# Kernel tuning notes

Measured on AMD Instinct MI355X. Metric: run time of the kernel, lower is better.

Reference implementation:

```python
import jax, jax.numpy as jnp
import numpy as np

STRIDE = 2
PADDING = 1


def setup_inputs() -> dict:
    key = jax.random.key(0)
    k1, k2, k3, k4, k5 = jax.random.split(key, 5)
    B, C, H, W = 32, 128, 64, 64
    O, kh, kw = 256, 3, 3
    ah = H + 2 * PADDING - (kh - 1)  # 64
    oh = ah // STRIDE                # 32 (divisible -> ceil == floor, rest == 0)
    inputs = {
        "input": jax.random.normal(k1, (B, C, H, W), dtype=jnp.float32),
        "weight": jax.random.normal(k2, (O, C, kh, kw), dtype=jnp.float32) * 0.05,
        "bias": jax.random.normal(k3, (O,), dtype=jnp.float32) * 0.05,
        "selh": jax.random.randint(k4, (oh, oh), 0, STRIDE, dtype=jnp.int32),
        "selw": jax.random.randint(k5, (oh, oh), 0, STRIDE, dtype=jnp.int32),
    }
    return inputs


def reference(input, weight, bias, selh, selw):
    # Faithful to SConv2dAvg.forward with stoch=True, mask == -1, stride=2:
    # unfold(input, k, pad, stride=1) -> stochastic gather of one position per
    # stride x stride cell (offsets selh/selw) -> GEMM with flattened weight -> reshape.
    B, C, H, W = input.shape
    O, _, kh, kw = weight.shape
    ah = H + 2 * PADDING - (kh - 1)
    aw = W + 2 * PADDING - (kw - 1)
    oh = ah // STRIDE  # divisible by construction; ceil_mode correction is a no-op
    ow = aw // STRIDE
    xp = jnp.pad(input, ((0, 0), (0, 0), (PADDING, PADDING), (PADDING, PADDING)))
    # selected unfold positions in the afterconv grid
    rng_h = selh + (jnp.arange(oh, dtype=selh.dtype) * STRIDE)[:, None]   # [oh, ow]
    rng_w = selw + (jnp.arange(ow, dtype=selw.dtype) * STRIDE)[None, :]   # [oh, ow]
    # gather k x k patches directly (equivalent to gathering unfold columns)
    rows = rng_h[:, :, None, None] + jnp.arange(kh)[None, None, :, None]  # [oh, ow, kh, 1]
    cols = rng_w[:, :, None, None] + jnp.arange(kw)[None, None, None, :]  # [oh, ow, 1, kw]
    patches = xp[:, :, rows, cols]  # [B, C, oh, ow, kh, kw]
    out = jnp.einsum('bchwij,ocij->bohw', patches, weight) + bias[None, :, None, None]
    return out  # [B, O, oh, ow]
```

## Files before the change

### kernel.cpp

```cpp
#include <hip/hip_runtime.h>
#include <hip/hip_bf16.h>


typedef short bf16x8 __attribute__((ext_vector_type(8)));
typedef float f32x4  __attribute__((ext_vector_type(4)));

#define KSTEPS 18
#define WPRE_BYTES (KSTEPS * 256 * 64 * 2)
#define TRANS_BYTES (32 * 66 * 66 * 128 * 2)
#define TOTAL_WS (WPRE_BYTES + TRANS_BYTES)

__device__ __forceinline__ unsigned short f2bf(float x) {
  unsigned u = __float_as_uint(x);
  return (unsigned short)((u + 0x7fffu + ((u >> 16) & 1u)) >> 16);
}
__device__ __forceinline__ unsigned pk2(float a, float b) {
  unsigned ua = __float_as_uint(a), ub = __float_as_uint(b);
  return ((ua + 0x7fffu + ((ua >> 16) & 1u)) >> 16) |
         ((ub + 0x7fffu + ((ub >> 16) & 1u)) & 0xffff0000u);
}
__device__ __forceinline__ bf16x8 ld_frag(const uint4* a) {
  union { uint4 u; bf16x8 s; } cv; cv.u = *a; return cv.s;
}
__device__ __forceinline__ void async16(const void* g, void* l) {
  __builtin_amdgcn_global_load_lds(
      (__attribute__((address_space(1))) void*)(void*)g,
      (__attribute__((address_space(3))) void*)l, 16, 0, 0);
}

__global__ __launch_bounds__(256) void wprep(const float* __restrict__ w,
                                             unsigned short* __restrict__ wpre) {
  int idx = (blockIdx.x << 8) + threadIdx.x;
  if (idx >= KSTEPS * 16384) return;
  int k_in = idx & 63;
  int o    = (idx >> 6) & 255;
  int kk   = idx >> 14;
  int kg   = (kk << 6) + (k_in ^ ((o & 7) << 3));
  int tap  = kg >> 7;
  int c    = kg & 127;
  int di   = (tap >= 6) ? 2 : ((tap >= 3) ? 1 : 0);
  int dj   = tap - di * 3;
  wpre[idx] = f2bf(w[(o * 128 + c) * 9 + di * 3 + dj]);
}

__global__ __launch_bounds__(256) void transform(const float* __restrict__ in,
                                                 unsigned short* __restrict__ tp) {
  __shared__ float lds[128 * 65];
  const int hp  = blockIdx.x;
  const int b   = blockIdx.y;
  const int tid = threadIdx.x;
  uint4* rowp = (uint4*)(tp + (size_t)(b * 66 + hp) * 66 * 128);
  uint4 z; z.x = z.y = z.z = z.w = 0u;
  if (hp == 0 || hp == 65) {
    for (int s = tid; s < 1056; s += 256) rowp[s] = z;
    return;
  }
  const int h = hp - 1;
  const float* src = in + ((size_t)b << 19) + (h << 6);
  const int w = tid & 63, c0 = tid >> 6;
#pragma unroll
  for (int pass = 0; pass < 32; ++pass) {
    int c = (pass << 2) + c0;
    lds[c * 65 + w] = src[((size_t)c << 12) + w];
  }
  __syncthreads();
  for (int s = tid; s < 1056; s += 256) {
    if (s < 16 || s >= 1040) { rowp[s] = z; continue; }
    int idx = s - 16;
    int wq = idx >> 4, c8 = idx & 15;
    const float* lp = lds + (c8 << 3) * 65 + wq;
    uint4 d;
    d.x = pk2(lp[0],   lp[65]);
    d.y = pk2(lp[130], lp[195]);
    d.z = pk2(lp[260], lp[325]);
    d.w = pk2(lp[390], lp[455]);
    rowp[s] = d;
  }
}

__global__ __launch_bounds__(512, 4) void sconv_mfma2(
    const unsigned short* __restrict__ tp,
    const unsigned short* __restrict__ wpre,
    const float* __restrict__ bias,
    const int* __restrict__ selh,
    const int* __restrict__ selw,
    float* __restrict__ out)
{
  __shared__ uint4 Alds[128 * 8];
  __shared__ uint4 Blds[128 * 8];
  __shared__ float bias_s[128];

  const int tid   = threadIdx.x;
  const int blk   = blockIdx.x;
  const int b     = blk >> 4;
  const int y0    = ((blk >> 1) & 7) << 2;
  const int ohalf = blk & 1;

  if (tid < 128) bias_s[tid] = bias[(ohalf << 7) + tid];

  const int p0 = tid >> 3;
  const int sl = tid & 7;
  int addr0, addr1;
  {
    const int py0 = y0 + (p0 >> 5);
    const int px  = p0 & 31;
    const int sh0 = selh[(py0 << 5) | px], sw0 = selw[(py0 << 5) | px];
    const int py1 = py0 + 2;
    const int sh1 = selh[(py1 << 5) | px], sw1 = selw[(py1 << 5) | px];
    addr0 = (b * 66 + 2 * py0 + sh0) * 66 + 2 * px + sw0;
    addr1 = (b * 66 + 2 * py1 + sh1) * 66 + 2 * px + sw1;
  }
  const int n0 = sl ^ (p0 & 7);
  const char* tbase = (const char*)tp;

  const int wv = tid >> 6, ln = tid & 63;
  const int wo = wv & 1;
  const int wp = wv >> 1;
  const int lo = ln & 15, hi = ln >> 4;

  const char* wsrc = (const char*)wpre + (ohalf << 14) + (tid << 4);

  f32x4 acc[4][2] = {};

  for (int kk = 0; kk < KSTEPS; ++kk) {
    const int tap = kk >> 1;
    const int di  = (tap >= 6) ? 2 : ((tap >= 3) ? 1 : 0);
    const int dj  = tap - 3 * di;
    const int toff = ((di * 66 + dj) << 8) + ((kk & 1) << 7) + (n0 << 4);

    async16(tbase + ((size_t)addr0 << 8) + toff, Alds + (wv << 6));
    async16(tbase + ((size_t)addr1 << 8) + toff, Alds + (wv << 6) + 512);
    async16(wsrc + (kk << 15),        Blds + (wv << 6));
    async16(wsrc + (kk << 15) + 8192, Blds + (wv << 6) + 512);

    __syncthreads();

    bf16x8 FW[4][2], FP[2][2];
#pragma unroll
    for (int f = 0; f < 4; ++f) {
      const int orow = (wo << 6) + (f << 4) + lo;
#pragma unroll
      for (int ks = 0; ks < 2; ++ks)
        FW[f][ks] = ld_frag(Blds + (orow << 3) + (((ks << 2) | hi) ^ (orow & 7)));
    }
#pragma unroll
    for (int f = 0; f < 2; ++f) {
      const int prow = (wp << 5) + (f << 4) + lo;
#pragma unroll
      for (int ks = 0; ks < 2; ++ks)
        FP[f][ks] = ld_frag(Alds + (prow << 3) + (((ks << 2) | hi) ^ (prow & 7)));
    }
#pragma unroll
    for (int fo = 0; fo < 4; ++fo)
#pragma unroll
      for (int fp = 0; fp < 2; ++fp)
#pragma unroll
        for (int ks = 0; ks < 2; ++ks)
          acc[fo][fp] = __builtin_amdgcn_mfma_f32_16x16x32_bf16(
              FW[fo][ks], FP[fp][ks], acc[fo][fp], 0, 0, 0);

    __syncthreads();
  }

  float* ob = out + ((size_t)b << 18) + ((size_t)ohalf << 17) + (y0 << 5);
#pragma unroll
  for (int fo = 0; fo < 4; ++fo) {
    const int obase = (wo << 6) + (fo << 4) + (hi << 2);
#pragma unroll
    for (int fp = 0; fp < 2; ++fp) {
      const int pix = (wp << 5) + (fp << 4) + lo;
#pragma unroll
      for (int j = 0; j < 4; ++j) {
        const int o = obase + j;
        ob[((size_t)o << 10) + pix] = acc[fo][fp][j] + bias_s[o];
      }
    }
  }
}

__global__ __launch_bounds__(512, 2) void sconv_mfma(
    const float* __restrict__ in, const unsigned short* __restrict__ wpre,
    const float* __restrict__ bias, const int* __restrict__ selh,
    const int* __restrict__ selw, float* __restrict__ out) {
  __shared__ uint4 Alds[128 * 8];
  __shared__ uint4 Blds[256 * 8];
  __shared__ float bias_s[256];
  const int tid = threadIdx.x;
  const int blk = blockIdx.x;
  const int b   = blk >> 3;
  const int y0  = (blk & 7) << 2;
  if (tid < 256) bias_s[tid] = bias[tid];
  const int p    = tid & 127;
  const int csub = tid >> 7;
  const int py   = y0 + (p >> 5);
  const int px   = p & 31;
  const int rh0  = 2 * py + selh[(py << 5) | px] - 1;
  const int rw0  = 2 * px + selw[(py << 5) | px] - 1;
  const float* inb = in + ((size_t)b << 19);
  const int wv = tid >> 6, ln = tid & 63;
  const int wo = wv & 3, wp = wv >> 2;
  const int lo = ln & 15, hi = ln >> 4;
  f32x4 acc[4][4] = {};
  for (int kk = 0; kk < KSTEPS; ++kk) {
    const int tap = kk >> 1;
    const int di  = (tap >= 6) ? 2 : ((tap >= 3) ? 1 : 0);
    const int dj  = tap - di * 3;
    const int rh  = rh0 + di;
    const int rw  = rw0 + dj;
    const bool ok = (rh >= 0) & (rh < 64) & (rw >= 0) & (rw < 64);
    {
      const char* gbase = (const char*)wpre + ((size_t)kk << 15);
#pragma unroll
      for (int r = 0; r < 4; ++r) {
        int chunk = (wv << 2) + r;
        async16(gbase + (chunk << 10) + (ln << 4), Blds + (chunk << 6));
      }
    }
    {
      const float* src = inb + ((size_t)(((kk & 1) << 6) + (csub << 4)) << 12)
                             + (rh << 6) + rw;
      float v[16];
#pragma unroll
      for (int cc = 0; cc < 16; ++cc)
        v[cc] = ok ? src[(size_t)cc << 12] : 0.f;
#pragma unroll
      for (int z = 0; z < 2; ++z) {
        uint4 d;
        d.x = pk2(v[z * 8 + 0], v[z * 8 + 1]);
        d.y = pk2(v[z * 8 + 2], v[z * 8 + 3]);
        d.z = pk2(v[z * 8 + 4], v[z * 8 + 5]);
        d.w = pk2(v[z * 8 + 6], v[z * 8 + 7]);
        int slot = ((csub << 1) | z) ^ (p & 7);
        Alds[(p << 3) + slot] = d;
      }
    }
    __syncthreads();
    bf16x8 FW[4][2], FP[4][2];
#pragma unroll
    for (int f = 0; f < 4; ++f) {
      const int orow = (wo << 6) + (f << 4) + lo;
      const int prow = (wp << 6) + (f << 4) + lo;
#pragma unroll
      for (int ks = 0; ks < 2; ++ks) {
        FW[f][ks] = ld_frag(Blds + (orow << 3) + (((ks << 2) | hi) ^ (orow & 7)));
        FP[f][ks] = ld_frag(Alds + (prow << 3) + (((ks << 2) | hi) ^ (prow & 7)));
      }
    }
#pragma unroll
    for (int fo = 0; fo < 4; ++fo)
#pragma unroll
      for (int fp = 0; fp < 4; ++fp)
#pragma unroll
        for (int ks = 0; ks < 2; ++ks)
          acc[fo][fp] = __builtin_amdgcn_mfma_f32_16x16x32_bf16(
              FW[fo][ks], FP[fp][ks], acc[fo][fp], 0, 0, 0);
    __syncthreads();
  }
  float* ob = out + ((size_t)b << 18) + (y0 << 5);
#pragma unroll
  for (int fo = 0; fo < 4; ++fo) {
    const int obase = (wo << 6) + (fo << 4) + (hi << 2);
#pragma unroll
    for (int fp = 0; fp < 4; ++fp) {
      const int pix = (wp << 6) + (fp << 4) + lo;
#pragma unroll
      for (int j = 0; j < 4; ++j) {
        const int o = obase + j;
        ob[((size_t)o << 10) + pix] = acc[fo][fp][j] + bias_s[o];
      }
    }
  }
}

__global__ __launch_bounds__(256) void sconv_naive(
    const float* __restrict__ in, const float* __restrict__ w,
    const float* __restrict__ bias, const int* __restrict__ selh,
    const int* __restrict__ selw, float* __restrict__ out) {
  int idx = (blockIdx.x << 8) + threadIdx.x;
  if (idx >= 32 * 256 * 32 * 32) return;
  int x = idx & 31, y = (idx >> 5) & 31, o = (idx >> 10) & 255, b = idx >> 18;
  int rh0 = 2 * y + selh[(y << 5) | x] - 1;
  int rw0 = 2 * x + selw[(y << 5) | x] - 1;
  const float* inb = in + ((size_t)b << 19);
  const float* wo_ = w + o * 1152;
  float acc = bias[o];
  for (int c = 0; c < 128; ++c)
    for (int i = 0; i < 3; ++i) {
      int rh = rh0 + i;
      if (rh < 0 || rh >= 64) continue;
      for (int j = 0; j < 3; ++j) {
        int rw = rw0 + j;
        if (rw < 0 || rw >= 64) continue;
        acc += inb[(c << 12) + (rh << 6) + rw] * wo_[c * 9 + i * 3 + j];
      }
    }
  out[idx] = acc;
}

extern "C" void kernel_launch(void* const* d_in, const int* in_sizes, int n_in,
                              void* d_out, int out_size, void* d_ws, size_t ws_size,
                              hipStream_t stream) {
  const float* in   = (const float*)d_in[0];
  const float* w    = (const float*)d_in[1];
  const float* bias = (const float*)d_in[2];
  const int*   selh = (const int*)d_in[3];
  const int*   selw = (const int*)d_in[4];
  float* out = (float*)d_out;

  if (ws_size >= (size_t)TOTAL_WS) {
    unsigned short* wpre = (unsigned short*)d_ws;
    unsigned short* tp   = (unsigned short*)((char*)d_ws + WPRE_BYTES);
    wprep<<<dim3(1152), dim3(256), 0, stream>>>(w, wpre);
    transform<<<dim3(66, 32), dim3(256), 0, stream>>>(in, tp);
    sconv_mfma2<<<dim3(512), dim3(512), 0, stream>>>(tp, wpre, bias, selh, selw, out);
  } else if (ws_size >= (size_t)WPRE_BYTES) {
    unsigned short* wpre = (unsigned short*)d_ws;
    wprep<<<dim3(1152), dim3(256), 0, stream>>>(w, wpre);
    sconv_mfma<<<dim3(256), dim3(512), 0, stream>>>(in, wpre, bias, selh, selw, out);
  } else {
    sconv_naive<<<dim3(32768), dim3(256), 0, stream>>>(in, w, bias, selh, selw, out);
  }
}
```

Before: 52.21 us.

## Double-buffer LDS in conv GEMM, fuse prep kernels, and remap block order

Merges the weight-prep and input-transform kernels into one launch, with extra grid columns doing the weight conversion, which removes a kernel launch. The main conv kernel now double-buffers its A/B LDS tiles: it issues async global-to-LDS loads for the next k-step before computing the current one, and uses explicit vmcnt/lgkmcnt waits with raw barriers. Block indices are permuted so that consecutive blocks map to different batches and tiles, which may change L2 locality. LDS use doubles, which may limit occupancy, and the hand-written waitcnt logic must stay correct.

```diff
diff --git a/kernel.cpp b/kernel.cpp
--- a/kernel.cpp
+++ b/kernel.cpp
@@ -28,27 +28,31 @@
       (__attribute__((address_space(3))) void*)l, 16, 0, 0);
 }
 
-__global__ __launch_bounds__(256) void wprep(const float* __restrict__ w,
-                                             unsigned short* __restrict__ wpre) {
-  int idx = (blockIdx.x << 8) + threadIdx.x;
-  if (idx >= KSTEPS * 16384) return;
-  int k_in = idx & 63;
-  int o    = (idx >> 6) & 255;
-  int kk   = idx >> 14;
-  int kg   = (kk << 6) + (k_in ^ ((o & 7) << 3));
-  int tap  = kg >> 7;
-  int c    = kg & 127;
-  int di   = (tap >= 6) ? 2 : ((tap >= 3) ? 1 : 0);
-  int dj   = tap - di * 3;
-  wpre[idx] = f2bf(w[(o * 128 + c) * 9 + di * 3 + dj]);
-}
-
-__global__ __launch_bounds__(256) void transform(const float* __restrict__ in,
-                                                 unsigned short* __restrict__ tp) {
+__global__ __launch_bounds__(256) void prep(const float* __restrict__ in,
+                                            const float* __restrict__ w,
+                                            unsigned short* __restrict__ tp,
+                                            unsigned short* __restrict__ wpre) {
+  const int tid = threadIdx.x;
+  if (blockIdx.x >= 66) {
+    const int kk = blockIdx.x - 66;
+    const int ob = blockIdx.y;
+#pragma unroll
+    for (int e = 0; e < 2; ++e) {
+      int t2   = (tid << 1) + e;
+      int o    = (ob << 3) + (t2 >> 6);
+      int k_in = t2 & 63;
+      int kg   = (kk << 6) + (k_in ^ ((o & 7) << 3));
+      int tap  = kg >> 7;
+      int c    = kg & 127;
+      int di   = (tap >= 6) ? 2 : ((tap >= 3) ? 1 : 0);
+      int dj   = tap - di * 3;
+      wpre[(kk << 14) + (o << 6) + k_in] = f2bf(w[(o * 128 + c) * 9 + di * 3 + dj]);
+    }
+    return;
+  }
   __shared__ float lds[128 * 65];
-  const int hp  = blockIdx.x;
-  const int b   = blockIdx.y;
-  const int tid = threadIdx.x;
+  const int hp = blockIdx.x;
+  const int b  = blockIdx.y;
   uint4* rowp = (uint4*)(tp + (size_t)(b * 66 + hp) * 66 * 128);
   uint4 z; z.x = z.y = z.z = z.w = 0u;
   if (hp == 0 || hp == 65) {
@@ -57,11 +61,11 @@
   }
   const int h = hp - 1;
   const float* src = in + ((size_t)b << 19) + (h << 6);
-  const int w = tid & 63, c0 = tid >> 6;
+  const int ww = tid & 63, c0 = tid >> 6;
 #pragma unroll
   for (int pass = 0; pass < 32; ++pass) {
     int c = (pass << 2) + c0;
-    lds[c * 65 + w] = src[((size_t)c << 12) + w];
+    lds[c * 65 + ww] = src[((size_t)c << 12) + ww];
   }
   __syncthreads();
   for (int s = tid; s < 1056; s += 256) {
@@ -78,7 +82,7 @@
   }
 }
 
-__global__ __launch_bounds__(512, 4) void sconv_mfma2(
+__global__ __launch_bounds__(512, 4) void sconv_mfma3(
     const unsigned short* __restrict__ tp,
     const unsigned short* __restrict__ wpre,
     const float* __restrict__ bias,
@@ -86,12 +90,13 @@
     const int* __restrict__ selw,
     float* __restrict__ out)
 {
-  __shared__ uint4 Alds[128 * 8];
-  __shared__ uint4 Blds[128 * 8];
+  __shared__ uint4 Alds[2][1024];
+  __shared__ uint4 Blds[2][1024];
   __shared__ float bias_s[128];
 
-  const int tid   = threadIdx.x;
-  const int blk   = blockIdx.x;
+  const int tid = threadIdx.x;
+  const int d    = blockIdx.x;
+  const int blk  = ((d & 7) << 6) + (d >> 3);
   const int b     = blk >> 4;
   const int y0    = ((blk >> 1) & 7) << 2;
   const int ohalf = blk & 1;
@@ -122,33 +127,49 @@
 
   f32x4 acc[4][2] = {};
 
+#define STAGE(BUF, KK)                                                        \
+  do {                                                                        \
+    const int tap_ = (KK) >> 1;                                               \
+    const int di_  = (tap_ >= 6) ? 2 : ((tap_ >= 3) ? 1 : 0);                 \
+    const int dj_  = tap_ - 3 * di_;                                          \
+    const int toff_ = ((di_ * 66 + dj_) << 8) + (((KK) & 1) << 7) + (n0 << 4);\
+    uint4* A_ = &Alds[BUF][0];                                                \
+    uint4* B_ = &Blds[BUF][0];                                                \
+    async16(tbase + ((size_t)addr0 << 8) + toff_, A_ + (wv << 6));            \
+    async16(tbase + ((size_t)addr1 << 8) + toff_, A_ + (wv << 6) + 512);      \
+    async16(wsrc + ((KK) << 15),        B_ + (wv << 6));                      \
+    async16(wsrc + ((KK) << 15) + 8192, B_ + (wv << 6) + 512);                \
+  } while (0)
+
+  STAGE(0, 0);
+  int cur = 0;
+
   for (int kk = 0; kk < KSTEPS; ++kk) {
-    const int tap = kk >> 1;
-    const int di  = (tap >= 6) ? 2 : ((tap >= 3) ? 1 : 0);
-    const int dj  = tap - 3 * di;
-    const int toff = ((di * 66 + dj) << 8) + ((kk & 1) << 7) + (n0 << 4);
-
-    async16(tbase + ((size_t)addr0 << 8) + toff, Alds + (wv << 6));
-    async16(tbase + ((size_t)addr1 << 8) + toff, Alds + (wv << 6) + 512);
-    async16(wsrc + (kk << 15),        Blds + (wv << 6));
-    async16(wsrc + (kk << 15) + 8192, Blds + (wv << 6) + 512);
-
-    __syncthreads();
-
+    if (kk < KSTEPS - 1) {
+      STAGE(cur ^ 1, kk + 1);
+      asm volatile("s_waitcnt vmcnt(4)" ::: "memory");
+    } else {
+      asm volatile("s_waitcnt vmcnt(0)" ::: "memory");
+    }
+    __builtin_amdgcn_s_barrier();
+    asm volatile("" ::: "memory");
+
+    const uint4* A = &Alds[cur][0];
+    const uint4* B = &Blds[cur][0];
     bf16x8 FW[4][2], FP[2][2];
 #pragma unroll
     for (int f = 0; f < 4; ++f) {
       const int orow = (wo << 6) + (f << 4) + lo;
 #pragma unroll
       for (int ks = 0; ks < 2; ++ks)
-        FW[f][ks] = ld_frag(Blds + (orow << 3) + (((ks << 2) | hi) ^ (orow & 7)));
+        FW[f][ks] = ld_frag(B + (orow << 3) + (((ks << 2) | hi) ^ (orow & 7)));
     }
 #pragma unroll
     for (int f = 0; f < 2; ++f) {
       const int prow = (wp << 5) + (f << 4) + lo;
 #pragma unroll
       for (int ks = 0; ks < 2; ++ks)
-        FP[f][ks] = ld_frag(Alds + (prow << 3) + (((ks << 2) | hi) ^ (prow & 7)));
+        FP[f][ks] = ld_frag(A + (prow << 3) + (((ks << 2) | hi) ^ (prow & 7)));
     }
 #pragma unroll
     for (int fo = 0; fo < 4; ++fo)
@@ -159,8 +180,12 @@
           acc[fo][fp] = __builtin_amdgcn_mfma_f32_16x16x32_bf16(
               FW[fo][ks], FP[fp][ks], acc[fo][fp], 0, 0, 0);
 
-    __syncthreads();
-  }
+    asm volatile("s_waitcnt lgkmcnt(0)" ::: "memory");
+    __builtin_amdgcn_s_barrier();
+    asm volatile("" ::: "memory");
+    cur ^= 1;
+  }
+#undef STAGE
 
   float* ob = out + ((size_t)b << 18) + ((size_t)ohalf << 17) + (y0 << 5);
 #pragma unroll
@@ -169,100 +194,6 @@
 #pragma unroll
     for (int fp = 0; fp < 2; ++fp) {
       const int pix = (wp << 5) + (fp << 4) + lo;
-#pragma unroll
-      for (int j = 0; j < 4; ++j) {
-        const int o = obase + j;
-        ob[((size_t)o << 10) + pix] = acc[fo][fp][j] + bias_s[o];
-      }
-    }
-  }
-}
-
-__global__ __launch_bounds__(512, 2) void sconv_mfma(
-    const float* __restrict__ in, const unsigned short* __restrict__ wpre,
-    const float* __restrict__ bias, const int* __restrict__ selh,
-    const int* __restrict__ selw, float* __restrict__ out) {
-  __shared__ uint4 Alds[128 * 8];
-  __shared__ uint4 Blds[256 * 8];
-  __shared__ float bias_s[256];
-  const int tid = threadIdx.x;
-  const int blk = blockIdx.x;
-  const int b   = blk >> 3;
-  const int y0  = (blk & 7) << 2;
-  if (tid < 256) bias_s[tid] = bias[tid];
-  const int p    = tid & 127;
-  const int csub = tid >> 7;
-  const int py   = y0 + (p >> 5);
-  const int px   = p & 31;
-  const int rh0  = 2 * py + selh[(py << 5) | px] - 1;
-  const int rw0  = 2 * px + selw[(py << 5) | px] - 1;
-  const float* inb = in + ((size_t)b << 19);
-  const int wv = tid >> 6, ln = tid & 63;
-  const int wo = wv & 3, wp = wv >> 2;
-  const int lo = ln & 15, hi = ln >> 4;
-  f32x4 acc[4][4] = {};
-  for (int kk = 0; kk < KSTEPS; ++kk) {
-    const int tap = kk >> 1;
-    const int di  = (tap >= 6) ? 2 : ((tap >= 3) ? 1 : 0);
-    const int dj  = tap - di * 3;
-    const int rh  = rh0 + di;
-    const int rw  = rw0 + dj;
-    const bool ok = (rh >= 0) & (rh < 64) & (rw >= 0) & (rw < 64);
-    {
-      const char* gbase = (const char*)wpre + ((size_t)kk << 15);
-#pragma unroll
-      for (int r = 0; r < 4; ++r) {
-        int chunk = (wv << 2) + r;
-        async16(gbase + (chunk << 10) + (ln << 4), Blds + (chunk << 6));
-      }
-    }
-    {
-      const float* src = inb + ((size_t)(((kk & 1) << 6) + (csub << 4)) << 12)
-                             + (rh << 6) + rw;
-      float v[16];
-#pragma unroll
-      for (int cc = 0; cc < 16; ++cc)
-        v[cc] = ok ? src[(size_t)cc << 12] : 0.f;
-#pragma unroll
-      for (int z = 0; z < 2; ++z) {
-        uint4 d;
-        d.x = pk2(v[z * 8 + 0], v[z * 8 + 1]);
-        d.y = pk2(v[z * 8 + 2], v[z * 8 + 3]);
-        d.z = pk2(v[z * 8 + 4], v[z * 8 + 5]);
-        d.w = pk2(v[z * 8 + 6], v[z * 8 + 7]);
-        int slot = ((csub << 1) | z) ^ (p & 7);
-        Alds[(p << 3) + slot] = d;
-      }
-    }
-    __syncthreads();
-    bf16x8 FW[4][2], FP[4][2];
-#pragma unroll
-    for (int f = 0; f < 4; ++f) {
-      const int orow = (wo << 6) + (f << 4) + lo;
-      const int prow = (wp << 6) + (f << 4) + lo;
-#pragma unroll
-      for (int ks = 0; ks < 2; ++ks) {
-        FW[f][ks] = ld_frag(Blds + (orow << 3) + (((ks << 2) | hi) ^ (orow & 7)));
-        FP[f][ks] = ld_frag(Alds + (prow << 3) + (((ks << 2) | hi) ^ (prow & 7)));
-      }
-    }
-#pragma unroll
-    for (int fo = 0; fo < 4; ++fo)
-#pragma unroll
-      for (int fp = 0; fp < 4; ++fp)
-#pragma unroll
-        for (int ks = 0; ks < 2; ++ks)
-          acc[fo][fp] = __builtin_amdgcn_mfma_f32_16x16x32_bf16(
-              FW[fo][ks], FP[fp][ks], acc[fo][fp], 0, 0, 0);
-    __syncthreads();
-  }
-  float* ob = out + ((size_t)b << 18) + (y0 << 5);
-#pragma unroll
-  for (int fo = 0; fo < 4; ++fo) {
-    const int obase = (wo << 6) + (fo << 4) + (hi << 2);
-#pragma unroll
-    for (int fp = 0; fp < 4; ++fp) {
-      const int pix = (wp << 6) + (fp << 4) + lo;
 #pragma unroll
       for (int j = 0; j < 4; ++j) {
         const int o = obase + j;
@@ -310,13 +241,8 @@
   if (ws_size >= (size_t)TOTAL_WS) {
     unsigned short* wpre = (unsigned short*)d_ws;
     unsigned short* tp   = (unsigned short*)((char*)d_ws + WPRE_BYTES);
-    wprep<<<dim3(1152), dim3(256), 0, stream>>>(w, wpre);
-    transform<<<dim3(66, 32), dim3(256), 0, stream>>>(in, tp);
-    sconv_mfma2<<<dim3(512), dim3(512), 0, stream>>>(tp, wpre, bias, selh, selw, out);
-  } else if (ws_size >= (size_t)WPRE_BYTES) {
-    unsigned short* wpre = (unsigned short*)d_ws;
-    wprep<<<dim3(1152), dim3(256), 0, stream>>>(w, wpre);
-    sconv_mfma<<<dim3(256), dim3(512), 0, stream>>>(in, wpre, bias, selh, selw, out);
+    prep<<<dim3(84, 32), dim3(256), 0, stream>>>(in, w, tp, wpre);
+    sconv_mfma3<<<dim3(512), dim3(512), 0, stream>>>(tp, wpre, bias, selh, selw, out);
   } else {
     sconv_naive<<<dim3(32768), dim3(256), 0, stream>>>(in, w, bias, selh, selw, out);
   }
```

Result: faster. 47.74 us (-8.6%).
